# Kernel tuning notes

Hardware: AMD Instinct MI355X
Metric: run time of the kernel (lower is better)

The kernel has to match this reference:

```python
import jax, jax.numpy as jnp
import numpy as np

NSEQ, T, OBS, ACT, H = 256, 1024, 128, 16, 64


def setup_inputs() -> dict:
    key = jax.random.key(0)
    ks = jax.random.split(key, 16)
    N = NSEQ * T
    obs = jax.random.normal(ks[0], (N, OBS), jnp.float32)
    action = jax.random.randint(ks[1], (N,), 0, ACT)
    ep = (jax.random.uniform(ks[2], (NSEQ, T)) < 0.02).astype(jnp.float32)
    ep = ep.at[:, 0].set(1.0)  # every padded sequence starts an episode
    episode_starts = ep.reshape(-1)
    z = lambda *s: jnp.zeros(s, jnp.float32)
    W = lambda k, shape, s=0.1: jax.random.normal(k, shape, jnp.float32) * s
    d = dict(
        obs=obs, action=action, episode_starts=episode_starts,
        h_pi=z(1, NSEQ, H), c_pi=z(1, NSEQ, H), h_vf=z(1, NSEQ, H), c_vf=z(1, NSEQ, H),
        Wp1=W(ks[3], (64, OBS)), bp1=z(64), Wp2=W(ks[4], (64, 64)), bp2=z(64),
        Wv1=W(ks[5], (64, OBS)), bv1=z(64), Wv2=W(ks[6], (64, 64)), bv2=z(64),
        Wih_pi=W(ks[7], (4 * H, 64)), Whh_pi=W(ks[8], (4 * H, H)), bih_pi=z(4 * H), bhh_pi=z(4 * H),
        Wih_vf=W(ks[9], (4 * H, 64)), Whh_vf=W(ks[10], (4 * H, H)), bih_vf=z(4 * H), bhh_vf=z(4 * H),
        Wa=W(ks[11], (ACT, H), 0.01), ba=z(ACT), Wc=W(ks[12], (1, H), 1.0), bc=z(1),
    )
    return d


def _mlp(x, W1, b1, W2, b2):
    # shared Linear->Tanh->Linear->Tanh feature extractor
    return jnp.tanh(jnp.tanh(x @ W1.T + b1) @ W2.T + b2)


def _lstm(feats, ep, h0, c0, Wih, Whh, bih, bhh):
    # feats: (NSEQ*T, 64) flattened as (n_seq, T); scan over time with episode-reset masking
    xs = feats.reshape(NSEQ, T, -1).transpose(1, 0, 2)  # (T, n_seq, 64)
    eps = ep.reshape(NSEQ, T).T                          # (T, n_seq)
    b = bih + bhh

    def step(carry, inp):
        h, c = carry
        x, e = inp
        m = (1.0 - e)[:, None]
        h = h * m
        c = c * m
        g = x @ Wih.T + h @ Whh.T + b                    # (n_seq, 4H), gate order i,f,g,o
        i, f, gg, o = jnp.split(g, 4, axis=-1)
        c = jax.nn.sigmoid(f) * c + jax.nn.sigmoid(i) * jnp.tanh(gg)
        h = jax.nn.sigmoid(o) * jnp.tanh(c)
        return (h, c), h

    _, outs = jax.lax.scan(step, (h0[0], c0[0]), (xs, eps))
    return outs.transpose(1, 0, 2).reshape(-1, H)        # (NSEQ*T, H)


def reference(obs, action, episode_starts, h_pi, c_pi, h_vf, c_vf,
              Wp1, bp1, Wp2, bp2, Wv1, bv1, Wv2, bv2,
              Wih_pi, Whh_pi, bih_pi, bhh_pi, Wih_vf, Whh_vf, bih_vf, bhh_vf,
              Wa, ba, Wc, bc):
    feat_pi = _mlp(obs, Wp1, bp1, Wp2, bp2)
    feat_vf = _mlp(obs, Wv1, bv1, Wv2, bv2)
    lat_pi = _lstm(feat_pi, episode_starts, h_pi, c_pi, Wih_pi, Whh_pi, bih_pi, bhh_pi)
    lat_vf = _lstm(feat_vf, episode_starts, h_vf, c_vf, Wih_vf, Whh_vf, bih_vf, bhh_vf)
    logits = lat_pi @ Wa.T + ba
    logp = jax.nn.log_softmax(logits, axis=-1)
    logprob = jnp.take_along_axis(logp, action[:, None], axis=-1)[:, 0]
    entropy = -jnp.sum(jnp.exp(logp) * logp, axis=-1)
    value = lat_vf @ Wc.T + bc
    return logprob, entropy, value
```

## Files before the change

kernel.cpp:

```cpp
#include <hip/hip_runtime.h>


#define NSEQ  256
#define TT    1024
#define NROWS (NSEQ * TT)
#define OBS   128
#define ACTN  16
#define HH    64

__device__ __forceinline__ float frcp(float x)  { return __builtin_amdgcn_rcpf(x); }
__device__ __forceinline__ float fsigm(float x) { return frcp(1.f + __expf(-x)); }
__device__ __forceinline__ float ftanh(float x) { return 1.f - 2.f * frcp(1.f + __expf(2.f * x)); }

__global__ void lstm_ac_zero(int* ctrs) {
    if (threadIdx.x < 2) ctrs[threadIdx.x] = 0;
}

__global__ void lstm_ac_episodes(const float* __restrict__ ep,
                                 int* __restrict__ ctrs, int2* __restrict__ eps) {
    __shared__ float flags[TT];
    const int s = blockIdx.x;
    for (int i = threadIdx.x; i < TT; i += blockDim.x) flags[i] = ep[(size_t)s * TT + i];
    __syncthreads();
    for (int t0 = threadIdx.x; t0 < TT; t0 += blockDim.x) {
        const bool start = (t0 == 0) || (flags[t0] > 0.5f);
        if (start) {
            int t1 = t0 + 1;
            while (t1 < TT && !(flags[t1] > 0.5f)) t1++;
            const int slot = atomicAdd(&ctrs[0], 1);
            eps[slot] = make_int2(s * TT + t0, t1 - t0);
        }
    }
}

__global__ __launch_bounds__(256) void lstm_ac_feat(
    const float* __restrict__ obs,
    const float* __restrict__ W1, const float* __restrict__ b1,
    const float* __restrict__ W2, const float* __restrict__ b2,
    float* __restrict__ feat) {
    __shared__ float x_lds[4][OBS];
    __shared__ float l1_lds[4][HH];
    const int tid = threadIdx.x;
    const int w = tid >> 6, j = tid & 63;

    float w1r[OBS], w2r[HH];
    {
        const float4* p1 = (const float4*)(W1 + (size_t)j * OBS);
#pragma unroll
        for (int q = 0; q < OBS / 4; q++) {
            float4 v = p1[q];
            w1r[4*q] = v.x; w1r[4*q+1] = v.y; w1r[4*q+2] = v.z; w1r[4*q+3] = v.w;
        }
        const float4* p2 = (const float4*)(W2 + (size_t)j * HH);
#pragma unroll
        for (int q = 0; q < HH / 4; q++) {
            float4 v = p2[q];
            w2r[4*q] = v.x; w2r[4*q+1] = v.y; w2r[4*q+2] = v.z; w2r[4*q+3] = v.w;
        }
    }
    const float bb1 = b1[j], bb2 = b2[j];
    const int gw = blockIdx.x * 4 + w;

    for (int rr = 0; rr < 64; ++rr) {
        const int r = gw * 64 + rr;
        x_lds[w][j]      = obs[(size_t)r * OBS + j];
        x_lds[w][HH + j] = obs[(size_t)r * OBS + HH + j];
        const float4* xv4 = (const float4*)x_lds[w];
        float sa[4] = {0.f, 0.f, 0.f, 0.f};
#pragma unroll
        for (int q = 0; q < OBS / 4; q++) {
            float4 v = xv4[q];
            sa[q & 3] += v.x * w1r[4*q] + v.y * w1r[4*q+1] + v.z * w1r[4*q+2] + v.w * w1r[4*q+3];
        }
        const float l1 = ftanh(bb1 + (sa[0] + sa[1]) + (sa[2] + sa[3]));
        l1_lds[w][j] = l1;
        const float4* lv4 = (const float4*)l1_lds[w];
        float ta[4] = {0.f, 0.f, 0.f, 0.f};
#pragma unroll
        for (int q = 0; q < HH / 4; q++) {
            float4 v = lv4[q];
            ta[q & 3] += v.x * w2r[4*q] + v.y * w2r[4*q+1] + v.z * w2r[4*q+2] + v.w * w2r[4*q+3];
        }
        feat[(size_t)r * HH + j] = ftanh(bb2 + (ta[0] + ta[1]) + (ta[2] + ta[3]));
    }
}

__global__ __launch_bounds__(256) void lstm_ac_scan(
    float* __restrict__ fl_pi, float* __restrict__ fl_vf,
    const float* __restrict__ Wih_pi, const float* __restrict__ Whh_pi,
    const float* __restrict__ bih_pi, const float* __restrict__ bhh_pi,
    const float* __restrict__ Wih_vf, const float* __restrict__ Whh_vf,
    const float* __restrict__ bih_vf, const float* __restrict__ bhh_vf,
    int* __restrict__ ctrs, const int2* __restrict__ eps) {
    __shared__ float h_lds[HH], c_lds[HH], x_lds[HH], g_lds[4 * HH];
    __shared__ int task_s;
    const int tid = threadIdx.x;
    const int w = tid >> 6, j = tid & 63;
    const int gidx = tid;
    const int ep_count = ctrs[0];
    const int ntasks = 2 * ep_count;

    int cur = -1;
    float wih[HH], whh[HH], bg = 0.f;
    float* fl = fl_pi;

    for (;;) {
        if (tid == 0) task_s = atomicAdd(&ctrs[1], 1);
        __syncthreads();
        const int task = task_s;
        if (task >= ntasks) break;
        const int l = (task >= ep_count) ? 1 : 0;
        if (l != cur) {
            cur = l;
            const float* Wih = l ? Wih_vf : Wih_pi;
            const float* Whh = l ? Whh_vf : Whh_pi;
            const float* bih = l ? bih_vf : bih_pi;
            const float* bhh = l ? bhh_vf : bhh_pi;
            fl = l ? fl_vf : fl_pi;
            const float4* p1 = (const float4*)(Wih + (size_t)gidx * HH);
            const float4* p2 = (const float4*)(Whh + (size_t)gidx * HH);
#pragma unroll
            for (int q = 0; q < HH / 4; q++) {
                float4 a = p1[q];
                wih[4*q] = a.x; wih[4*q+1] = a.y; wih[4*q+2] = a.z; wih[4*q+3] = a.w;
                float4 b = p2[q];
                whh[4*q] = b.x; whh[4*q+1] = b.y; whh[4*q+2] = b.z; whh[4*q+3] = b.w;
            }
            bg = bih[gidx] + bhh[gidx];
        }
        const int2 e = eps[(task >= ep_count) ? (task - ep_count) : task];
        const int r0 = e.x, len = e.y;

        if (w == 0) { h_lds[j] = 0.f; c_lds[j] = 0.f; }
        if (w == 1 && j < 16)
            ((float4*)x_lds)[j] = ((const float4*)(fl + (size_t)r0 * HH))[j];
        __syncthreads();

        for (int t = 0; t < len; ++t) {
            float a0 = bg, a1 = 0.f, a2 = 0.f, a3 = 0.f;
            const float4* hv4 = (const float4*)h_lds;
            const float4* xv4 = (const float4*)x_lds;
#pragma unroll
            for (int q = 0; q < HH / 4; q++) {
                float4 hv = hv4[q];
                float4 xv = xv4[q];
                float p = hv.x * whh[4*q] + hv.y * whh[4*q+1] + hv.z * whh[4*q+2] + hv.w * whh[4*q+3]
                        + xv.x * wih[4*q] + xv.y * wih[4*q+1] + xv.z * wih[4*q+2] + xv.w * wih[4*q+3];
                if ((q & 3) == 0) a0 += p; else if ((q & 3) == 1) a1 += p;
                else if ((q & 3) == 2) a2 += p; else a3 += p;
            }
            const float g = (a0 + a1) + (a2 + a3);
            g_lds[gidx] = (w == 2) ? ftanh(g) : fsigm(g);
            __syncthreads();
            if (w == 0) {
                float c = g_lds[HH + j] * c_lds[j] + g_lds[j] * g_lds[2 * HH + j];
                float h = g_lds[3 * HH + j] * ftanh(c);
                c_lds[j] = c;
                h_lds[j] = h;
                fl[(size_t)(r0 + t) * HH + j] = h;
            } else if (w == 1 && j < 16 && (t + 1) < len) {
                ((float4*)x_lds)[j] = ((const float4*)(fl + (size_t)(r0 + t + 1) * HH))[j];
            }
            __syncthreads();
        }
    }
}

__global__ __launch_bounds__(256) void lstm_ac_heads(
    const float* __restrict__ lat_pi, const float* __restrict__ lat_vf,
    const int* __restrict__ action,
    const float* __restrict__ Wa, const float* __restrict__ ba,
    const float* __restrict__ Wc, const float* __restrict__ bc,
    float* __restrict__ out) {
    const int r = blockIdx.x * 256 + threadIdx.x;
    float4 lp[16];
    const float4* pp = (const float4*)(lat_pi + (size_t)r * HH);
#pragma unroll
    for (int q = 0; q < 16; q++) lp[q] = pp[q];

    float logits[ACTN];
#pragma unroll
    for (int a = 0; a < ACTN; a++) {
        const float4* wp = (const float4*)(Wa + (size_t)a * HH);
        float s0 = 0.f, s1 = 0.f, s2 = 0.f, s3 = 0.f;
#pragma unroll
        for (int q = 0; q < 16; q++) {
            float4 wv = wp[q];
            s0 += lp[q].x * wv.x; s1 += lp[q].y * wv.y;
            s2 += lp[q].z * wv.z; s3 += lp[q].w * wv.w;
        }
        logits[a] = ba[a] + (s0 + s1) + (s2 + s3);
    }
    float m = logits[0];
#pragma unroll
    for (int a = 1; a < ACTN; a++) m = fmaxf(m, logits[a]);
    float s0 = 0.f, s1 = 0.f;
#pragma unroll
    for (int a = 0; a < ACTN; a++) {
        const float e = __expf(logits[a] - m);
        s0 += e;
        s1 += e * logits[a];
    }
    const float lse = m + __logf(s0);
    const int act = action[r];
    float la = logits[0];
#pragma unroll
    for (int a = 1; a < ACTN; a++) la = (act == a) ? logits[a] : la;
    out[r] = la - lse;
    out[NROWS + r] = lse - s1 * frcp(s0);

    const float4* pv = (const float4*)(lat_vf + (size_t)r * HH);
    const float4* wc4 = (const float4*)Wc;
    float t0 = 0.f, t1 = 0.f, t2 = 0.f, t3 = 0.f;
#pragma unroll
    for (int q = 0; q < 16; q++) {
        float4 v = pv[q];
        float4 wv = wc4[q];
        t0 += v.x * wv.x; t1 += v.y * wv.y; t2 += v.z * wv.z; t3 += v.w * wv.w;
    }
    out[2 * (size_t)NROWS + r] = bc[0] + (t0 + t1) + (t2 + t3);
}

extern "C" void kernel_launch(void* const* d_in, const int* in_sizes, int n_in,
                              void* d_out, int out_size, void* d_ws, size_t ws_size,
                              hipStream_t stream) {
    const float* obs    = (const float*)d_in[0];
    const int*   action = (const int*)d_in[1];
    const float* epst   = (const float*)d_in[2];
    const float* Wp1 = (const float*)d_in[7];
    const float* bp1 = (const float*)d_in[8];
    const float* Wp2 = (const float*)d_in[9];
    const float* bp2 = (const float*)d_in[10];
    const float* Wv1 = (const float*)d_in[11];
    const float* bv1 = (const float*)d_in[12];
    const float* Wv2 = (const float*)d_in[13];
    const float* bv2 = (const float*)d_in[14];
    const float* Wih_pi = (const float*)d_in[15];
    const float* Whh_pi = (const float*)d_in[16];
    const float* bih_pi = (const float*)d_in[17];
    const float* bhh_pi = (const float*)d_in[18];
    const float* Wih_vf = (const float*)d_in[19];
    const float* Whh_vf = (const float*)d_in[20];
    const float* bih_vf = (const float*)d_in[21];
    const float* bhh_vf = (const float*)d_in[22];
    const float* Wa = (const float*)d_in[23];
    const float* ba = (const float*)d_in[24];
    const float* Wc = (const float*)d_in[25];
    const float* bc = (const float*)d_in[26];
    float* out = (float*)d_out;

    char* ws = (char*)d_ws;
    int*  ctrs = (int*)ws;
    int2* eps  = (int2*)(ws + 256);
    float* fl_pi = (float*)(ws + 256 + (size_t)NROWS * sizeof(int2));
    float* fl_vf = fl_pi + (size_t)NROWS * HH;

    lstm_ac_zero<<<1, 64, 0, stream>>>(ctrs);
    lstm_ac_episodes<<<NSEQ, 256, 0, stream>>>(epst, ctrs, eps);
    lstm_ac_feat<<<NROWS / 256, 256, 0, stream>>>(obs, Wp1, bp1, Wp2, bp2, fl_pi);
    lstm_ac_feat<<<NROWS / 256, 256, 0, stream>>>(obs, Wv1, bv1, Wv2, bv2, fl_vf);
    lstm_ac_scan<<<2048, 256, 0, stream>>>(fl_pi, fl_vf,
                                           Wih_pi, Whh_pi, bih_pi, bhh_pi,
                                           Wih_vf, Whh_vf, bih_vf, bhh_vf,
                                           ctrs, eps);
    lstm_ac_heads<<<NROWS / 256, 256, 0, stream>>>(fl_pi, fl_vf, action,
                                                   Wa, ba, Wc, bc, out);
}
```

Measured before the change: 2.147 ms.

## Sort episodes by length and batch four per LSTM scan block

Builds a length histogram, a descending prefix sum and a scatter so that episodes are sorted from longest to shortest. The scan kernel then handles four similar-length episodes per 512-thread block, with each gate row split across two lanes and combined by a shuffle, and it keeps the cell state in registers. This is meant to amortise per-step barriers and weight registers over several sequences and to balance dynamic scheduling by starting long episodes first. It adds three small kernels and some lanes idle while episode lengths differ; the feature kernel also gets more blocks and an occupancy hint.

```diff
diff --git a/kernel.cpp b/kernel.cpp
--- a/kernel.cpp
+++ b/kernel.cpp
@@ -7,17 +7,21 @@
 #define OBS   128
 #define ACTN  16
 #define HH    64
+#define MAXEP NROWS
 
 __device__ __forceinline__ float frcp(float x)  { return __builtin_amdgcn_rcpf(x); }
 __device__ __forceinline__ float fsigm(float x) { return frcp(1.f + __expf(-x)); }
 __device__ __forceinline__ float ftanh(float x) { return 1.f - 2.f * frcp(1.f + __expf(2.f * x)); }
 
-__global__ void lstm_ac_zero(int* ctrs) {
-    if (threadIdx.x < 2) ctrs[threadIdx.x] = 0;
+__global__ void lstm_ac_zero(int* ctrs, int* hist) {
+    const int t = threadIdx.x;
+    hist[t] = 0;
+    if (t < 8) ctrs[t] = 0;
 }
 
 __global__ void lstm_ac_episodes(const float* __restrict__ ep,
-                                 int* __restrict__ ctrs, int2* __restrict__ eps) {
+                                 int* __restrict__ ctrs, int* __restrict__ hist,
+                                 int2* __restrict__ raw) {
     __shared__ float flags[TT];
     const int s = blockIdx.x;
     for (int i = threadIdx.x; i < TT; i += blockDim.x) flags[i] = ep[(size_t)s * TT + i];
@@ -27,13 +31,40 @@
         if (start) {
             int t1 = t0 + 1;
             while (t1 < TT && !(flags[t1] > 0.5f)) t1++;
+            const int len = t1 - t0;
             const int slot = atomicAdd(&ctrs[0], 1);
-            eps[slot] = make_int2(s * TT + t0, t1 - t0);
-        }
-    }
-}
-
-__global__ __launch_bounds__(256) void lstm_ac_feat(
+            raw[slot] = make_int2(s * TT + t0, len);
+            atomicAdd(&hist[len - 1], 1);
+        }
+    }
+}
+
+__global__ void lstm_ac_prefix(const int* __restrict__ hist, int* __restrict__ offs) {
+    __shared__ int a[1024];
+    const int tid = threadIdx.x;
+    const int h0 = hist[tid];
+    a[tid] = h0;
+    __syncthreads();
+    for (int s = 1; s < 1024; s <<= 1) {
+        const int v = (tid + s < 1024) ? a[tid + s] : 0;
+        __syncthreads();
+        a[tid] += v;
+        __syncthreads();
+    }
+    offs[tid] = a[tid] - h0;
+}
+
+__global__ void lstm_ac_scatter(const int* __restrict__ ctrs, const int2* __restrict__ raw,
+                                int* __restrict__ offs, int2* __restrict__ sorted) {
+    const int i = blockIdx.x * 256 + threadIdx.x;
+    if (i < ctrs[0]) {
+        const int2 e = raw[i];
+        const int slot = atomicAdd(&offs[e.y - 1], 1);
+        sorted[slot] = e;
+    }
+}
+
+__global__ __launch_bounds__(256, 2) void lstm_ac_feat(
     const float* __restrict__ obs,
     const float* __restrict__ W1, const float* __restrict__ b1,
     const float* __restrict__ W2, const float* __restrict__ b2,
@@ -61,8 +92,8 @@
     const float bb1 = b1[j], bb2 = b2[j];
     const int gw = blockIdx.x * 4 + w;
 
-    for (int rr = 0; rr < 64; ++rr) {
-        const int r = gw * 64 + rr;
+    for (int rr = 0; rr < 32; ++rr) {
+        const int r = gw * 32 + rr;
         x_lds[w][j]      = obs[(size_t)r * OBS + j];
         x_lds[w][HH + j] = obs[(size_t)r * OBS + HH + j];
         const float4* xv4 = (const float4*)x_lds[w];
@@ -85,81 +116,120 @@
     }
 }
 
-__global__ __launch_bounds__(256) void lstm_ac_scan(
+__global__ __launch_bounds__(512, 3) void lstm_ac_scan(
     float* __restrict__ fl_pi, float* __restrict__ fl_vf,
     const float* __restrict__ Wih_pi, const float* __restrict__ Whh_pi,
     const float* __restrict__ bih_pi, const float* __restrict__ bhh_pi,
     const float* __restrict__ Wih_vf, const float* __restrict__ Whh_vf,
     const float* __restrict__ bih_vf, const float* __restrict__ bhh_vf,
-    int* __restrict__ ctrs, const int2* __restrict__ eps) {
-    __shared__ float h_lds[HH], c_lds[HH], x_lds[HH], g_lds[4 * HH];
+    int* __restrict__ ctrs, const int2* __restrict__ sorted) {
+    __shared__ float x_lds[4][HH];
+    __shared__ float h_lds[4][HH];
+    __shared__ float g_lds[4][4 * HH];
     __shared__ int task_s;
+
     const int tid = threadIdx.x;
-    const int w = tid >> 6, j = tid & 63;
-    const int gidx = tid;
-    const int ep_count = ctrs[0];
-    const int ntasks = 2 * ep_count;
+    const int w   = tid >> 6;
+    const int l   = tid & 63;
+    const int g   = (w << 5) + (l >> 1);
+    const int kh  = l & 1;
+    const int kbase = kh * 32;
+    const bool upd = (w < 4);
+    const int b_me = upd ? w : (w - 4);
+    const int j = l;
+    const bool is_tanh_gate = ((w >> 1) == 2);
+
+    const int cnt = ctrs[0];
+    const int G = (cnt + 3) >> 2;
+    const int ntasks = 2 * G;
 
     int cur = -1;
-    float wih[HH], whh[HH], bg = 0.f;
+    float wih[32], whh[32];
+    float bg = 0.f;
     float* fl = fl_pi;
+    float c_reg = 0.f;
 
     for (;;) {
+        __syncthreads();
         if (tid == 0) task_s = atomicAdd(&ctrs[1], 1);
         __syncthreads();
         const int task = task_s;
         if (task >= ntasks) break;
-        const int l = (task >= ep_count) ? 1 : 0;
-        if (l != cur) {
-            cur = l;
-            const float* Wih = l ? Wih_vf : Wih_pi;
-            const float* Whh = l ? Whh_vf : Whh_pi;
-            const float* bih = l ? bih_vf : bih_pi;
-            const float* bhh = l ? bhh_vf : bhh_pi;
-            fl = l ? fl_vf : fl_pi;
-            const float4* p1 = (const float4*)(Wih + (size_t)gidx * HH);
-            const float4* p2 = (const float4*)(Whh + (size_t)gidx * HH);
-#pragma unroll
-            for (int q = 0; q < HH / 4; q++) {
+        const int lstm = (task >= G) ? 1 : 0;
+        const int gq = lstm ? (task - G) : task;
+        if (lstm != cur) {
+            cur = lstm;
+            const float* Wih = lstm ? Wih_vf : Wih_pi;
+            const float* Whh = lstm ? Whh_vf : Whh_pi;
+            const float* bih = lstm ? bih_vf : bih_pi;
+            const float* bhh = lstm ? bhh_vf : bhh_pi;
+            fl = lstm ? fl_vf : fl_pi;
+            const float4* p1 = (const float4*)(Wih + (size_t)g * HH + kbase);
+            const float4* p2 = (const float4*)(Whh + (size_t)g * HH + kbase);
+#pragma unroll
+            for (int q = 0; q < 8; q++) {
                 float4 a = p1[q];
-                wih[4*q] = a.x; wih[4*q+1] = a.y; wih[4*q+2] = a.z; wih[4*q+3] = a.w;
+                wih[4*q+0] = a.x; wih[4*q+1] = a.y; wih[4*q+2] = a.z; wih[4*q+3] = a.w;
                 float4 b = p2[q];
-                whh[4*q] = b.x; whh[4*q+1] = b.y; whh[4*q+2] = b.z; whh[4*q+3] = b.w;
+                whh[4*q+0] = b.x; whh[4*q+1] = b.y; whh[4*q+2] = b.z; whh[4*q+3] = b.w;
             }
-            bg = bih[gidx] + bhh[gidx];
-        }
-        const int2 e = eps[(task >= ep_count) ? (task - ep_count) : task];
-        const int r0 = e.x, len = e.y;
-
-        if (w == 0) { h_lds[j] = 0.f; c_lds[j] = 0.f; }
-        if (w == 1 && j < 16)
-            ((float4*)x_lds)[j] = ((const float4*)(fl + (size_t)r0 * HH))[j];
-        __syncthreads();
-
-        for (int t = 0; t < len; ++t) {
-            float a0 = bg, a1 = 0.f, a2 = 0.f, a3 = 0.f;
-            const float4* hv4 = (const float4*)h_lds;
-            const float4* xv4 = (const float4*)x_lds;
-#pragma unroll
-            for (int q = 0; q < HH / 4; q++) {
-                float4 hv = hv4[q];
-                float4 xv = xv4[q];
-                float p = hv.x * whh[4*q] + hv.y * whh[4*q+1] + hv.z * whh[4*q+2] + hv.w * whh[4*q+3]
-                        + xv.x * wih[4*q] + xv.y * wih[4*q+1] + xv.z * wih[4*q+2] + xv.w * wih[4*q+3];
-                if ((q & 3) == 0) a0 += p; else if ((q & 3) == 1) a1 += p;
-                else if ((q & 3) == 2) a2 += p; else a3 += p;
+            bg = (kh == 0) ? (bih[g] + bhh[g]) : 0.f;
+        }
+
+        int r0[4], ln[4];
+#pragma unroll
+        for (int s = 0; s < 4; s++) {
+            const int idx = gq * 4 + s;
+            if (idx < cnt) { const int2 e = sorted[idx]; r0[s] = e.x; ln[s] = e.y; }
+            else { r0[s] = 0; ln[s] = 0; }
+        }
+        const int maxlen = ln[0];
+
+        if (upd) { h_lds[b_me][j] = 0.f; c_reg = 0.f; }
+        else if (ln[b_me] > 0) x_lds[b_me][j] = fl[(size_t)r0[b_me] * HH + j];
+        __syncthreads();
+
+        for (int t = 0; t < maxlen; ++t) {
+            float xnext = 0.f;
+            if (!upd) {
+                const int tn = t + 1;
+                const int rr = (tn < ln[b_me]) ? (r0[b_me] + tn) : r0[b_me];
+                xnext = fl[(size_t)rr * HH + j];
             }
-            const float g = (a0 + a1) + (a2 + a3);
-            g_lds[gidx] = (w == 2) ? ftanh(g) : fsigm(g);
+#pragma unroll
+            for (int b = 0; b < 4; b++) {
+                if (t < ln[b]) {
+                    const float4* xv = (const float4*)&x_lds[b][kbase];
+                    const float4* hv = (const float4*)&h_lds[b][kbase];
+                    float a0 = bg, a1 = 0.f, a2 = 0.f, a3 = 0.f;
+#pragma unroll
+                    for (int q = 0; q < 8; q++) {
+                        const float4 x4 = xv[q];
+                        const float4 h4 = hv[q];
+                        a0 += x4.x * wih[4*q+0] + h4.x * whh[4*q+0];
+                        a1 += x4.y * wih[4*q+1] + h4.y * whh[4*q+1];
+                        a2 += x4.z * wih[4*q+2] + h4.z * whh[4*q+2];
+                        a3 += x4.w * wih[4*q+3] + h4.w * whh[4*q+3];
+                    }
+                    float part = (a0 + a1) + (a2 + a3);
+                    part += __shfl_xor(part, 1, 64);
+                    g_lds[b][g] = is_tanh_gate ? ftanh(part) : fsigm(part);
+                }
+            }
             __syncthreads();
-            if (w == 0) {
-                float c = g_lds[HH + j] * c_lds[j] + g_lds[j] * g_lds[2 * HH + j];
-                float h = g_lds[3 * HH + j] * ftanh(c);
-                c_lds[j] = c;
-                h_lds[j] = h;
-                fl[(size_t)(r0 + t) * HH + j] = h;
-            } else if (w == 1 && j < 16 && (t + 1) < len) {
-                ((float4*)x_lds)[j] = ((const float4*)(fl + (size_t)(r0 + t + 1) * HH))[j];
+            if (upd) {
+                if (t < ln[b_me]) {
+                    const float gi = g_lds[b_me][j];
+                    const float gf = g_lds[b_me][HH + j];
+                    const float gg = g_lds[b_me][2 * HH + j];
+                    const float go = g_lds[b_me][3 * HH + j];
+                    c_reg = gf * c_reg + gi * gg;
+                    const float h = go * ftanh(c_reg);
+                    h_lds[b_me][j] = h;
+                    fl[(size_t)(r0[b_me] + t) * HH + j] = h;
+                }
+            } else {
+                if (t + 1 < ln[b_me]) x_lds[b_me][j] = xnext;
             }
             __syncthreads();
         }
@@ -185,7 +255,7 @@
         float s0 = 0.f, s1 = 0.f, s2 = 0.f, s3 = 0.f;
 #pragma unroll
         for (int q = 0; q < 16; q++) {
-            float4 wv = wp[q];
+            const float4 wv = wp[q];
             s0 += lp[q].x * wv.x; s1 += lp[q].y * wv.y;
             s2 += lp[q].z * wv.z; s3 += lp[q].w * wv.w;
         }
@@ -214,8 +284,8 @@
     float t0 = 0.f, t1 = 0.f, t2 = 0.f, t3 = 0.f;
 #pragma unroll
     for (int q = 0; q < 16; q++) {
-        float4 v = pv[q];
-        float4 wv = wc4[q];
+        const float4 v = pv[q];
+        const float4 wv = wc4[q];
         t0 += v.x * wv.x; t1 += v.y * wv.y; t2 += v.z * wv.z; t3 += v.w * wv.w;
     }
     out[2 * (size_t)NROWS + r] = bc[0] + (t0 + t1) + (t2 + t3);
@@ -250,19 +320,24 @@
     float* out = (float*)d_out;
 
     char* ws = (char*)d_ws;
-    int*  ctrs = (int*)ws;
-    int2* eps  = (int2*)(ws + 256);
-    float* fl_pi = (float*)(ws + 256 + (size_t)NROWS * sizeof(int2));
+    int*  ctrs   = (int*)ws;
+    int*  hist   = (int*)(ws + 32);
+    int*  offs   = (int*)(ws + 32 + 4096);
+    int2* raw    = (int2*)(ws + 32 + 8192);
+    int2* sorted = raw + MAXEP;
+    float* fl_pi = (float*)((char*)(sorted + MAXEP));
     float* fl_vf = fl_pi + (size_t)NROWS * HH;
 
-    lstm_ac_zero<<<1, 64, 0, stream>>>(ctrs);
-    lstm_ac_episodes<<<NSEQ, 256, 0, stream>>>(epst, ctrs, eps);
-    lstm_ac_feat<<<NROWS / 256, 256, 0, stream>>>(obs, Wp1, bp1, Wp2, bp2, fl_pi);
-    lstm_ac_feat<<<NROWS / 256, 256, 0, stream>>>(obs, Wv1, bv1, Wv2, bv2, fl_vf);
-    lstm_ac_scan<<<2048, 256, 0, stream>>>(fl_pi, fl_vf,
+    lstm_ac_zero<<<1, 1024, 0, stream>>>(ctrs, hist);
+    lstm_ac_episodes<<<NSEQ, 256, 0, stream>>>(epst, ctrs, hist, raw);
+    lstm_ac_feat<<<2048, 256, 0, stream>>>(obs, Wp1, bp1, Wp2, bp2, fl_pi);
+    lstm_ac_feat<<<2048, 256, 0, stream>>>(obs, Wv1, bv1, Wv2, bv2, fl_vf);
+    lstm_ac_prefix<<<1, 1024, 0, stream>>>(hist, offs);
+    lstm_ac_scatter<<<1024, 256, 0, stream>>>(ctrs, raw, offs, sorted);
+    lstm_ac_scan<<<1024, 512, 0, stream>>>(fl_pi, fl_vf,
                                            Wih_pi, Whh_pi, bih_pi, bhh_pi,
                                            Wih_vf, Whh_vf, bih_vf, bhh_vf,
-                                           ctrs, eps);
+                                           ctrs, sorted);
     lstm_ac_heads<<<NROWS / 256, 256, 0, stream>>>(fl_pi, fl_vf, action,
                                                    Wa, ba, Wc, bc, out);
 }
```

Result: faster. 1.907 ms (-11.2%).
